# Kernel tuning notes

Hardware: AMD Instinct MI355X
Metric: run time of the kernel (lower is better)

Reference implementation:

```python
import jax, jax.numpy as jnp
import numpy as np

B, L = 64, 2048
V, E, G = 30, 128, 8          # n_tokens, embedding_size, n_globals
C, F, O = 64, 128, 30         # res_channels, f_channels, n_outputs
K, ND = 2, 9                  # kernel_size, n_dilations
GE = G * E                    # flattened global embedding dim


def causal_conv(x, w, b, dilation):
    # x: [B,Cin,L], w: [Cout,Cin,K] -> [B,Cout,L], causal via left padding
    pad = (w.shape[-1] - 1) * dilation
    out = jax.lax.conv_general_dilated(
        x, w, window_strides=(1,), padding=[(pad, 0)],
        rhs_dilation=(dilation,), dimension_numbers=("NCH", "OIH", "NCH"))
    return out + b[None, :, None]


def setup_inputs() -> dict:
    key = jax.random.key(0)
    ks = jax.random.split(key, 20)
    s = 0.05
    inp = {
        "input_tensor": jax.random.randint(ks[0], (B, L), 0, V),
        "global_input": jax.random.randint(ks[1], (B, G), 0, V),
        "emb_table": jax.random.normal(ks[2], (V, E), jnp.float32) * s,
        "w_causal": jax.random.normal(ks[3], (C, E, K), jnp.float32) * s,
        "b_causal": jnp.zeros((C,), jnp.float32),
        "w_f": jax.random.normal(ks[4], (ND, C, C, K), jnp.float32) * s,
        "b_f": jnp.zeros((ND, C), jnp.float32),
        "w_g": jax.random.normal(ks[5], (ND, C, C, K), jnp.float32) * s,
        "b_g": jnp.zeros((ND, C), jnp.float32),
        "wl_f": jax.random.normal(ks[6], (ND, C, GE), jnp.float32) * s,
        "bl_f": jnp.zeros((ND, C), jnp.float32),
        "wl_g": jax.random.normal(ks[7], (ND, C, GE), jnp.float32) * s,
        "bl_g": jnp.zeros((ND, C), jnp.float32),
        "w_res": jax.random.normal(ks[8], (ND, C, C), jnp.float32) * s,
        "b_res": jnp.zeros((ND, C), jnp.float32),
        "w_fin1": jax.random.normal(ks[9], (F, C), jnp.float32) * s,
        "b_fin1": jnp.zeros((F,), jnp.float32),
        "w_fin2": jax.random.normal(ks[10], (O, F), jnp.float32) * s,
        "b_fin2": jnp.zeros((O,), jnp.float32),
    }
    return inp


def reference(input_tensor, global_input, emb_table, w_causal, b_causal,
              w_f, b_f, w_g, b_g, wl_f, bl_f, wl_g, bl_g,
              w_res, b_res, w_fin1, b_fin1, w_fin2, b_fin2):
    # padding_idx=0: row 0 is zero and receives no gradient
    table = emb_table.at[0].set(0.0)
    emb = table[input_tensor]                     # [B,L,E]
    emb_g = table[global_input].reshape(B, GE)    # [B,G*E]
    x = jnp.transpose(emb, (0, 2, 1))             # [B,E,L]
    res = causal_conv(x, w_causal, b_causal, 1)   # [B,C,L]
    skips = jnp.zeros_like(res)
    for i in range(ND):
        d = 2 ** (i + 1)
        h_f = emb_g @ wl_f[i].T + bl_f[i]         # [B,C]
        h_g = emb_g @ wl_g[i].T + bl_g[i]
        x_f = causal_conv(res, w_f[i], b_f[i], d) + h_f[:, :, None]
        x_g = causal_conv(res, w_g[i], b_g[i], d) + h_g[:, :, None]
        z = jnp.tanh(x_f) * jax.nn.sigmoid(x_g)   # gated activation
        skip = jnp.einsum("oc,bcl->bol", w_res[i], z) + b_res[i][None, :, None]
        res = res + skip
        skips = skips + skip
    out = jax.nn.relu(skips)
    out = jnp.einsum("fc,bcl->bfl", w_fin1, out) + b_fin1[None, :, None]
    out = jax.nn.relu(out)
    out = jnp.einsum("of,bfl->bol", w_fin2, out) + b_fin2[None, :, None]
    return out
```

## Files before the change

### kernel.cpp

```cpp
#include <hip/hip_runtime.h>
#include <stdint.h>

#define Bz 64
#define Lz 2048
#define Vz 30
#define Ez 128
#define Gz 8
#define Cz 64
#define Fz 128
#define Oz 30
#define NDz 9

typedef __attribute__((ext_vector_type(8))) short short8;
typedef __attribute__((ext_vector_type(4))) float floatx4;

#define MFMA16 __builtin_amdgcn_mfma_f32_16x16x32_bf16

__device__ __forceinline__ uint16_t f2bf(float f) {
    uint32_t u = __float_as_uint(f);
    u += 0x7fffu + ((u >> 16) & 1u);
    return (uint16_t)(u >> 16);
}
__device__ __forceinline__ uint32_t bfround(float f) {
    uint32_t u = __float_as_uint(f);
    return u + 0x7fffu + ((u >> 16) & 1u);
}
__device__ __forceinline__ uint32_t pack2(float lo, float hi) {
    return __builtin_amdgcn_perm(bfround(hi), bfround(lo), 0x07060302u);
}
__device__ __forceinline__ float bf2f(uint32_t u) {
    return __uint_as_float(u << 16);
}
__device__ __forceinline__ float gatefn(float f, float g) {
    float a = __expf(2.f * f);
    float b = __expf(-g);
    float ap1 = a + 1.f;
    return (a - 1.f) * __builtin_amdgcn_rcpf(fmaf(ap1, b, ap1));
}

#define N_WB   (NDz * 128 * 128)
#define N_WR   (NDz * 64 * 64)
#define N_W1   (Fz * Cz)
#define N_W2   (32 * Fz)
#define N_PROJ (Vz * Cz)
#define N_WLB  (NDz * 128 * 1024)
#define N_EMB  (Bz * 1024)
#define N_BIAS (NDz * 128)

__global__ void pack_k(const float* __restrict__ w_f, const float* __restrict__ w_g,
                       const float* __restrict__ w_res, const float* __restrict__ w_fin1,
                       const float* __restrict__ w_fin2, const float* __restrict__ w_causal,
                       const float* __restrict__ table, const int* __restrict__ gin,
                       const float* __restrict__ wl_f, const float* __restrict__ wl_g,
                       const float* __restrict__ b_f, const float* __restrict__ b_g,
                       const float* __restrict__ bl_f, const float* __restrict__ bl_g,
                       uint16_t* __restrict__ WB, uint16_t* __restrict__ WrB,
                       uint16_t* __restrict__ W1B, uint16_t* __restrict__ W2B,
                       float* __restrict__ proj0, float* __restrict__ proj1,
                       uint16_t* __restrict__ WLB, uint16_t* __restrict__ embG,
                       float* __restrict__ biasrow) {
    int tid = blockIdx.x * 256 + threadIdx.x;
    if (tid < N_WB) {
        int i = tid >> 14, rem = tid & 16383, ch = rem >> 7, k = rem & 127;
        int kin = k & 63, tap = (k < 64) ? 1 : 0;
        float v = (ch < 64) ? w_f[((i * Cz + ch) * Cz + kin) * 2 + tap]
                            : w_g[((i * Cz + (ch - 64)) * Cz + kin) * 2 + tap];
        WB[tid] = f2bf(v);
        return;
    }
    tid -= N_WB;
    if (tid < N_WR) { WrB[tid] = f2bf(w_res[tid]); return; }
    tid -= N_WR;
    if (tid < N_W1) { W1B[tid] = f2bf(w_fin1[tid]); return; }
    tid -= N_W1;
    if (tid < N_W2) {
        int o = tid >> 7, f = tid & 127;
        W2B[tid] = f2bf(o < Oz ? w_fin2[o * Fz + f] : 0.f);
        return;
    }
    tid -= N_W2;
    if (tid < N_PROJ) {
        int v = tid >> 6, c = tid & 63;
        float s0 = 0.f, s1 = 0.f;
        if (v != 0) {
            for (int e = 0; e < Ez; e++) {
                float tv = table[v * Ez + e];
                s0 += w_causal[(c * Ez + e) * 2 + 0] * tv;
                s1 += w_causal[(c * Ez + e) * 2 + 1] * tv;
            }
        }
        proj0[tid] = s0; proj1[tid] = s1;
        return;
    }
    tid -= N_PROJ;
    if (tid < N_WLB) {
        int row = tid >> 10, j = tid & 1023;
        int i = row >> 7, rem = row & 127, fg = rem >> 6, c = rem & 63;
        const float* wl = fg ? wl_g : wl_f;
        WLB[tid] = f2bf(wl[((size_t)(i * Cz + c)) * 1024 + j]);
        return;
    }
    tid -= N_WLB;
    if (tid < N_EMB) {
        int b = tid >> 10, j = tid & 1023;
        int g = j >> 7, e = j & 127;
        int v = gin[b * Gz + g];
        embG[tid] = f2bf(v ? table[v * Ez + e] : 0.f);
        return;
    }
    tid -= N_EMB;
    if (tid < N_BIAS) {
        int i = tid >> 7, rem = tid & 127, fg = rem >> 6, c = rem & 63;
        biasrow[tid] = (fg ? b_g : b_f)[i * Cz + c] + (fg ? bl_g : bl_f)[i * Cz + c];
    }
}

__global__ __launch_bounds__(256) void hgemm_k(
    const uint16_t* __restrict__ WLB, const uint16_t* __restrict__ embG,
    const float* __restrict__ biasrow, float* __restrict__ hhT) {
    int tx = threadIdx.x, lane = tx & 63, wave = tx >> 6;
    int nl = lane & 15, quad = lane >> 4;
    int row0 = blockIdx.x * 64 + wave * 16;
    floatx4 acc[4];
    float bv[4];
#pragma unroll
    for (int r = 0; r < 4; r++) bv[r] = biasrow[row0 + quad * 4 + r];
#pragma unroll
    for (int nt = 0; nt < 4; nt++)
#pragma unroll
        for (int r = 0; r < 4; r++) acc[nt][r] = bv[r];
    const uint16_t* ap = WLB + (size_t)(row0 + nl) * 1024 + quad * 8;
#pragma unroll 4
    for (int ks = 0; ks < 32; ks++) {
        short8 a = *(const short8*)(ap + ks * 32);
#pragma unroll
        for (int nt = 0; nt < 4; nt++) {
            short8 bb = *(const short8*)(embG + (size_t)(nt * 16 + nl) * 1024 + ks * 32 + quad * 8);
            acc[nt] = MFMA16(a, bb, acc[nt], 0, 0, 0);
        }
    }
#pragma unroll
    for (int nt = 0; nt < 4; nt++)
#pragma unroll
        for (int r = 0; r < 4; r++)
            hhT[(size_t)(row0 + quad * 4 + r) * 64 + nt * 16 + nl] = acc[nt][r];
}

__global__ __launch_bounds__(256) void init_k(
    const int* __restrict__ tok, const float* __restrict__ b_causal,
    const float* __restrict__ proj0, const float* __restrict__ proj1,
    uint16_t* __restrict__ res) {
    int tx = threadIdx.x;
    int q = tx & 15, tl = tx >> 4;
    int b = blockIdx.y;
    int t = blockIdx.x * 16 + tl;
    int v1 = tok[b * Lz + t];
    int v0 = (t > 0) ? tok[b * Lz + t - 1] : 0;
    float4 p1 = ((const float4*)(proj1 + v1 * Cz))[q];
    float4 p0 = ((const float4*)(proj0 + v0 * Cz))[q];
    float4 bc = ((const float4*)b_causal)[q];
    float rx = p1.x + p0.x + bc.x, ry = p1.y + p0.y + bc.y;
    float rz = p1.z + p0.z + bc.z, rw = p1.w + p0.w + bc.w;
    *(uint2*)(res + ((size_t)(b * Lz + t)) * Cz + q * 4) =
        make_uint2(pack2(rx, ry), pack2(rz, rw));
}

__global__ __launch_bounds__(256, 2) void fused_k(
    const uint16_t* __restrict__ rin, uint16_t* __restrict__ rout,
    const uint16_t* __restrict__ WB, const uint16_t* __restrict__ WrB,
    const float* __restrict__ hhT, const float* __restrict__ b_res) {
    __shared__ __align__(16) uint16_t R[256 * 72];
    __shared__ __align__(16) uint16_t Zb[256 * 72];
    int tx = threadIdx.x;
    int lane = tx & 63, wave = tx >> 6;
    int nl = lane & 15, quad = lane >> 4;
    int b = blockIdx.y, t0 = blockIdx.x * 128;
    const uint16_t* rb16 = rin + ((size_t)b * Lz) * Cz;

    if (t0 != 0) {
        const uint16_t* src = rb16 + (size_t)(t0 - 128) * Cz;
#pragma unroll
        for (int it = 0; it < 8; it++) {
            int id = it * 256 + tx, row = id >> 3, c8 = id & 7;
            uint4 v = *(const uint4*)(src + (size_t)row * Cz + c8 * 8);
            *(uint4*)(R + row * 72 + c8 * 8) = v;
        }
    } else {
#pragma unroll
        for (int it = 0; it < 8; it++) {
            int id = it * 256 + tx, row = id >> 3, c8 = id & 7;
            int t = row - 128;
            uint4 v = make_uint4(0u, 0u, 0u, 0u);
            if (t >= 0) v = *(const uint4*)(rb16 + (size_t)t * Cz + c8 * 8);
            *(uint4*)(R + row * 72 + c8 * 8) = v;
        }
    }
    floatx4 ss[8];
#pragma unroll
    for (int j = 0; j < 8; j++)
#pragma unroll
        for (int r = 0; r < 4; r++) ss[j][r] = 0.f;
    __syncthreads();

    const int chq = wave * 16 + quad * 4;
    const int NT0[6] = {0, 0, 0, 1, 3, 7};

#pragma unroll
    for (int l = 0; l < 6; l++) {
        const int d = 2 << l;
        const int nt0 = NT0[l];
        const uint16_t* wf = WB + l * 16384 + (wave * 16 + nl) * 128 + quad * 8;
        short8 AF[4], AG[4];
#pragma unroll
        for (int ks = 0; ks < 4; ks++) {
            AF[ks] = *(const short8*)(wf + ks * 32);
            AG[ks] = *(const short8*)(wf + 64 * 128 + ks * 32);
        }
        const uint16_t* wr = WrB + l * 4096 + (wave * 16 + nl) * 64 + quad * 8;
        short8 AR0 = *(const short8*)(wr);
        short8 AR1 = *(const short8*)(wr + 32);
        float hfv[4], hgv[4], brv[4];
        const float* hp = hhT + ((size_t)(l * 128 + wave * 16 + quad * 4)) * 64 + b;
#pragma unroll
        for (int r = 0; r < 4; r++) { hfv[r] = hp[r * 64]; hgv[r] = hp[4096 + r * 64]; }
        const float* brp = b_res + l * Cz + wave * 16 + quad * 4;
#pragma unroll
        for (int r = 0; r < 4; r++) brv[r] = brp[r];

#pragma unroll
        for (int nt = 0; nt < 16; nt++) {
            if (nt < nt0) continue;
            int rowa = nt * 16 + nl;
            int rowb = rowa - d; rowb = rowb < 0 ? 0 : rowb;
            const uint16_t* ra = R + rowa * 72 + quad * 8;
            const uint16_t* rb = R + rowb * 72 + quad * 8;
            short8 b0 = *(const short8*)(ra);
            short8 b1 = *(const short8*)(ra + 32);
            short8 b2 = *(const short8*)(rb);
            short8 b3 = *(const short8*)(rb + 32);
            floatx4 aF, aG;
#pragma unroll
            for (int r = 0; r < 4; r++) { aF[r] = hfv[r]; aG[r] = hgv[r]; }
            aF = MFMA16(AF[0], b0, aF, 0, 0, 0); aG = MFMA16(AG[0], b0, aG, 0, 0, 0);
            aF = MFMA16(AF[1], b1, aF, 0, 0, 0); aG = MFMA16(AG[1], b1, aG, 0, 0, 0);
            aF = MFMA16(AF[2], b2, aF, 0, 0, 0); aG = MFMA16(AG[2], b2, aG, 0, 0, 0);
            aF = MFMA16(AF[3], b3, aF, 0, 0, 0); aG = MFMA16(AG[3], b3, aG, 0, 0, 0);
            float z0 = gatefn(aF[0], aG[0]);
            float z1 = gatefn(aF[1], aG[1]);
            float z2 = gatefn(aF[2], aG[2]);
            float z3 = gatefn(aF[3], aG[3]);
            *(uint2*)(Zb + rowa * 72 + chq) = make_uint2(pack2(z0, z1), pack2(z2, z3));
        }
        __syncthreads();

        if (t0 != 0) {
#pragma unroll
            for (int nt = 0; nt < 16; nt++) {
                if (nt < nt0) continue;
                int pos = nt * 16 + nl;
                const uint16_t* zp = Zb + pos * 72 + quad * 8;
                floatx4 a2;
#pragma unroll
                for (int r = 0; r < 4; r++) a2[r] = brv[r];
                a2 = MFMA16(AR0, *(const short8*)zp, a2, 0, 0, 0);
                a2 = MFMA16(AR1, *(const short8*)(zp + 32), a2, 0, 0, 0);
                uint16_t* rp = R + pos * 72 + chq;
                uint2 oldp = *(uint2*)rp;
                float n0 = bf2f(oldp.x & 0xffffu) + a2[0];
                float n1 = bf2f(oldp.x >> 16) + a2[1];
                float n2 = bf2f(oldp.y & 0xffffu) + a2[2];
                float n3 = bf2f(oldp.y >> 16) + a2[3];
                *(uint2*)rp = make_uint2(pack2(n0, n1), pack2(n2, n3));
                if (nt >= 8) {
#pragma unroll
                    for (int r = 0; r < 4; r++) ss[nt - 8][r] += a2[r];
                }
            }
        } else {
#pragma unroll
            for (int nt = 0; nt < 16; nt++) {
                if (nt < nt0) continue;
                int pos = nt * 16 + nl;
                const uint16_t* zp = Zb + pos * 72 + quad * 8;
                floatx4 a2;
#pragma unroll
                for (int r = 0; r < 4; r++) a2[r] = brv[r];
                a2 = MFMA16(AR0, *(const short8*)zp, a2, 0, 0, 0);
                a2 = MFMA16(AR1, *(const short8*)(zp + 32), a2, 0, 0, 0);
                int t = pos - 128;
                uint16_t* rp = R + pos * 72 + chq;
                uint2 oldp = *(uint2*)rp;
                bool ok = (t >= 0);
                float n0 = ok ? bf2f(oldp.x & 0xffffu) + a2[0] : 0.f;
                float n1 = ok ? bf2f(oldp.x >> 16) + a2[1] : 0.f;
                float n2 = ok ? bf2f(oldp.y & 0xffffu) + a2[2] : 0.f;
                float n3 = ok ? bf2f(oldp.y >> 16) + a2[3] : 0.f;
                *(uint2*)rp = make_uint2(pack2(n0, n1), pack2(n2, n3));
                if (nt >= 8) {
#pragma unroll
                    for (int r = 0; r < 4; r++) ss[nt - 8][r] += a2[r];
                }
            }
        }
        __syncthreads();
    }

    uint16_t* ro = rout + ((size_t)b * Lz) * Cz;
#pragma unroll
    for (int j = 0; j < 8; j++) {
        size_t off = (size_t)(t0 + j * 16 + nl) * Cz + chq;
        uint2 rv = *(const uint2*)(rb16 + off);
        float n0 = bf2f(rv.x & 0xffffu) + ss[j][0];
        float n1 = bf2f(rv.x >> 16) + ss[j][1];
        float n2 = bf2f(rv.y & 0xffffu) + ss[j][2];
        float n3 = bf2f(rv.y >> 16) + ss[j][3];
        *(uint2*)(ro + off) = make_uint2(pack2(n0, n1), pack2(n2, n3));
    }
}

__global__ __launch_bounds__(256, 4) void layer_k(
    const uint16_t* __restrict__ rin, uint16_t* __restrict__ rout,
    const uint16_t* __restrict__ WBl, const uint16_t* __restrict__ WrBl,
    const float* __restrict__ hhT, const float* __restrict__ b_res,
    int i, int d) {
    __shared__ __align__(16) uint16_t X[64 * 136];
    __shared__ __align__(16) uint16_t Z[64 * 72];
    int tx = threadIdx.x;
    int lane = tx & 63, wave = tx >> 6;
    int nl = lane & 15, quad = lane >> 4;
    int b = blockIdx.y, t0 = blockIdx.x * 64;
    const uint16_t* rb16 = rin + ((size_t)b * Lz) * Cz;

#pragma unroll
    for (int it = 0; it < 2; it++) {
        int id = it * 256 + tx, row = id >> 3, c8 = id & 7;
        uint4 v = *(const uint4*)(rb16 + (size_t)(t0 + row) * Cz + c8 * 8);
        *(uint4*)(X + row * 136 + c8 * 8) = v;
    }
#pragma unroll
    for (int it = 0; it < 2; it++) {
        int id = it * 256 + tx, row = id >> 3, c8 = id & 7;
        int tb = t0 + row - d;
        uint4 v = make_uint4(0u, 0u, 0u, 0u);
        if (tb >= 0) v = *(const uint4*)(rb16 + (size_t)tb * Cz + c8 * 8);
        *(uint4*)(X + row * 136 + 64 + c8 * 8) = v;
    }

    short8 AF[4], AG[4], AR[2];
    {
        const uint16_t* wf = WBl + (wave * 16 + nl) * 128 + quad * 8;
#pragma unroll
        for (int ks = 0; ks < 4; ks++) {
            AF[ks] = *(const short8*)(wf + ks * 32);
            AG[ks] = *(const short8*)(wf + 64 * 128 + ks * 32);
        }
        const uint16_t* wr = WrBl + (wave * 16 + nl) * 64 + quad * 8;
#pragma unroll
        for (int ks = 0; ks < 2; ks++) AR[ks] = *(const short8*)(wr + ks * 32);
    }
    float hfv[4], hgv[4], brv[4];
    {
        const float* hp = hhT + ((size_t)(i * 128 + wave * 16 + quad * 4)) * 64 + b;
#pragma unroll
        for (int r = 0; r < 4; r++) {
            hfv[r] = hp[r * 64];
            hgv[r] = hp[4096 + r * 64];
        }
        const float* brp = b_res + i * Cz + wave * 16 + quad * 4;
#pragma unroll
        for (int r = 0; r < 4; r++) brv[r] = brp[r];
    }
    __syncthreads();

    floatx4 accF[4], accG[4];
#pragma unroll
    for (int nt = 0; nt < 4; nt++)
#pragma unroll
        for (int r = 0; r < 4; r++) { accF[nt][r] = hfv[r]; accG[nt][r] = hgv[r]; }
#pragma unroll
    for (int nt = 0; nt < 4; nt++) {
        const uint16_t* xp = X + (nt * 16 + nl) * 136 + quad * 8;
#pragma unroll
        for (int ks = 0; ks < 4; ks++) {
            short8 bf = *(const short8*)(xp + ks * 32);
            accF[nt] = MFMA16(AF[ks], bf, accF[nt], 0, 0, 0);
            accG[nt] = MFMA16(AG[ks], bf, accG[nt], 0, 0, 0);
        }
    }

    int chq = wave * 16 + quad * 4;
#pragma unroll
    for (int nt = 0; nt < 4; nt++) {
        int pos = nt * 16 + nl;
        float z0 = gatefn(accF[nt][0], accG[nt][0]);
        float z1 = gatefn(accF[nt][1], accG[nt][1]);
        float z2 = gatefn(accF[nt][2], accG[nt][2]);
        float z3 = gatefn(accF[nt][3], accG[nt][3]);
        *(uint2*)(Z + pos * 72 + chq) = make_uint2(pack2(z0, z1), pack2(z2, z3));
    }
    __syncthreads();

    floatx4 acc2[4];
#pragma unroll
    for (int nt = 0; nt < 4; nt++)
#pragma unroll
        for (int r = 0; r < 4; r++) acc2[nt][r] = brv[r];
#pragma unroll
    for (int nt = 0; nt < 4; nt++) {
        const uint16_t* zp = Z + (nt * 16 + nl) * 72 + quad * 8;
        acc2[nt] = MFMA16(AR[0], *(const short8*)zp, acc2[nt], 0, 0, 0);
        acc2[nt] = MFMA16(AR[1], *(const short8*)(zp + 32), acc2[nt], 0, 0, 0);
    }

    uint16_t* ro = rout + ((size_t)b * Lz) * Cz;
#pragma unroll
    for (int nt = 0; nt < 4; nt++) {
        size_t off = (size_t)(t0 + nt * 16 + nl) * Cz + chq;
        uint2 rv = *(const uint2*)(rb16 + off);
        float n0 = bf2f(rv.x & 0xffffu) + acc2[nt][0];
        float n1 = bf2f(rv.x >> 16) + acc2[nt][1];
        float n2 = bf2f(rv.y & 0xffffu) + acc2[nt][2];
        float n3 = bf2f(rv.y >> 16) + acc2[nt][3];
        *(uint2*)(ro + off) = make_uint2(pack2(n0, n1), pack2(n2, n3));
    }
}

__global__ __launch_bounds__(256, 3) void final_k(
    const uint16_t* __restrict__ res0, const uint16_t* __restrict__ resF,
    const uint16_t* __restrict__ W1B, const uint16_t* __restrict__ W2B,
    const float* __restrict__ b_fin1, const float* __restrict__ b_fin2,
    float* __restrict__ out) {
    __shared__ __align__(16) uint16_t S[128 * 72];
    __shared__ __align__(16) uint16_t Mi[128 * 136];
    int tx = threadIdx.x;
    int lane = tx & 63, wave = tx >> 6;
    int nl = lane & 15, quad = lane >> 4;
    int b = blockIdx.y, t0 = blockIdx.x * 128;
    const uint16_t* r0 = res0 + ((size_t)b * Lz) * Cz;
    const uint16_t* rF = resF + ((size_t)b * Lz) * Cz;

    short8 A1[2][2], A2[2][4];
#pragma unroll
    for (int mt = 0; mt < 2; mt++) {
        const uint16_t* w1 = W1B + (wave * 32 + mt * 16 + nl) * 64 + quad * 8;
#pragma unroll
        for (int ks = 0; ks < 2; ks++) A1[mt][ks] = *(const short8*)(w1 + ks * 32);
        const uint16_t* w2 = W2B + (mt * 16 + nl) * 128 + quad * 8;
#pragma unroll
        for (int ks = 0; ks < 4; ks++) A2[mt][ks] = *(const short8*)(w2 + ks * 32);
    }
#pragma unroll
    for (int it = 0; it < 4; it++) {
        int id = it * 256 + tx, row = id >> 3, c8 = id & 7;
        uint4 fv = *(const uint4*)(rF + (size_t)(t0 + row) * Cz + c8 * 8);
        uint4 ov = *(const uint4*)(r0 + (size_t)(t0 + row) * Cz + c8 * 8);
        float s0 = fmaxf(bf2f(fv.x & 0xffffu) - bf2f(ov.x & 0xffffu), 0.f);
        float s1 = fmaxf(bf2f(fv.x >> 16) - bf2f(ov.x >> 16), 0.f);
        float s2 = fmaxf(bf2f(fv.y & 0xffffu) - bf2f(ov.y & 0xffffu), 0.f);
        float s3 = fmaxf(bf2f(fv.y >> 16) - bf2f(ov.y >> 16), 0.f);
        float s4 = fmaxf(bf2f(fv.z & 0xffffu) - bf2f(ov.z & 0xffffu), 0.f);
        float s5 = fmaxf(bf2f(fv.z >> 16) - bf2f(ov.z >> 16), 0.f);
        float s6 = fmaxf(bf2f(fv.w & 0xffffu) - bf2f(ov.w & 0xffffu), 0.f);
        float s7 = fmaxf(bf2f(fv.w >> 16) - bf2f(ov.w >> 16), 0.f);
        *(uint4*)(S + row * 72 + c8 * 8) =
            make_uint4(pack2(s0, s1), pack2(s2, s3), pack2(s4, s5), pack2(s6, s7));
    }
    __syncthreads();

    floatx4 accM[2][8];
    float b1v[2][4];
#pragma unroll
    for (int mt = 0; mt < 2; mt++)
#pragma unroll
        for (int r = 0; r < 4; r++) b1v[mt][r] = b_fin1[wave * 32 + mt * 16 + quad * 4 + r];
#pragma unroll
    for (int mt = 0; mt < 2; mt++)
#pragma unroll
        for (int nt = 0; nt < 8; nt++)
#pragma unroll
            for (int r = 0; r < 4; r++) accM[mt][nt][r] = b1v[mt][r];
#pragma unroll
    for (int nt = 0; nt < 8; nt++) {
        const uint16_t* sp = S + (nt * 16 + nl) * 72 + quad * 8;
#pragma unroll
        for (int ks = 0; ks < 2; ks++) {
            short8 s = *(const short8*)(sp + ks * 32);
            accM[0][nt] = MFMA16(A1[0][ks], s, accM[0][nt], 0, 0, 0);
            accM[1][nt] = MFMA16(A1[1][ks], s, accM[1][nt], 0, 0, 0);
        }
    }
#pragma unroll
    for (int mt = 0; mt < 2; mt++)
#pragma unroll
        for (int nt = 0; nt < 8; nt++) {
            int pos = nt * 16 + nl;
            int fq = wave * 32 + mt * 16 + quad * 4;
            float m0 = fmaxf(accM[mt][nt][0], 0.f), m1 = fmaxf(accM[mt][nt][1], 0.f);
            float m2 = fmaxf(accM[mt][nt][2], 0.f), m3 = fmaxf(accM[mt][nt][3], 0.f);
            *(uint2*)(Mi + pos * 136 + fq) = make_uint2(pack2(m0, m1), pack2(m2, m3));
        }
    __syncthreads();

    floatx4 accO[2][2];
#pragma unroll
    for (int mt = 0; mt < 2; mt++)
#pragma unroll
        for (int r = 0; r < 4; r++) {
            int o = mt * 16 + quad * 4 + r;
            float bo = (o < Oz) ? b_fin2[o] : 0.f;
            accO[mt][0][r] = bo; accO[mt][1][r] = bo;
        }
#pragma unroll
    for (int ntl = 0; ntl < 2; ntl++) {
        int nt = wave * 2 + ntl;
        const uint16_t* mp = Mi + (nt * 16 + nl) * 136 + quad * 8;
#pragma unroll
        for (int ks = 0; ks < 4; ks++) {
            short8 m = *(const short8*)(mp + ks * 32);
            accO[0][ntl] = MFMA16(A2[0][ks], m, accO[0][ntl], 0, 0, 0);
            accO[1][ntl] = MFMA16(A2[1][ks], m, accO[1][ntl], 0, 0, 0);
        }
    }
#pragma unroll
    for (int mt = 0; mt < 2; mt++)
#pragma unroll
        for (int ntl = 0; ntl < 2; ntl++)
#pragma unroll
            for (int r = 0; r < 4; r++) {
                int o = mt * 16 + quad * 4 + r;
                if (o < Oz)
                    out[((size_t)b * Oz + o) * Lz + t0 + (wave * 2 + ntl) * 16 + nl] =
                        accO[mt][ntl][r];
            }
}

extern "C" void kernel_launch(void* const* d_in, const int* in_sizes, int n_in,
                              void* d_out, int out_size, void* d_ws, size_t ws_size,
                              hipStream_t stream) {
    const int*   tok      = (const int*)d_in[0];
    const int*   gin      = (const int*)d_in[1];
    const float* table    = (const float*)d_in[2];
    const float* w_causal = (const float*)d_in[3];
    const float* b_causal = (const float*)d_in[4];
    const float* w_f      = (const float*)d_in[5];
    const float* b_f      = (const float*)d_in[6];
    const float* w_g      = (const float*)d_in[7];
    const float* b_g      = (const float*)d_in[8];
    const float* wl_f     = (const float*)d_in[9];
    const float* bl_f     = (const float*)d_in[10];
    const float* wl_g     = (const float*)d_in[11];
    const float* bl_g     = (const float*)d_in[12];
    const float* w_res    = (const float*)d_in[13];
    const float* b_res    = (const float*)d_in[14];
    const float* w_fin1   = (const float*)d_in[15];
    const float* b_fin1   = (const float*)d_in[16];
    const float* w_fin2   = (const float*)d_in[17];
    const float* b_fin2   = (const float*)d_in[18];
    float* out = (float*)d_out;

    const size_t NRES = (size_t)Bz * Lz * Cz;
    uint16_t* u16 = (uint16_t*)d_ws;
    uint16_t* resA = u16;
    uint16_t* resB = resA + NRES;
    uint16_t* resC = resB + NRES;
    uint16_t* WB   = resC + NRES;
    uint16_t* WrB  = WB + N_WB;
    uint16_t* W1B  = WrB + N_WR;
    uint16_t* W2B  = W1B + N_W1;
    uint16_t* WLB  = W2B + N_W2;
    uint16_t* embG = WLB + N_WLB;
    float* hhT     = (float*)(embG + N_EMB);
    float* proj0   = hhT + 73728;
    float* proj1   = proj0 + N_PROJ;
    float* biasrow = proj1 + N_PROJ;

    int npack = N_WB + N_WR + N_W1 + N_W2 + N_PROJ + N_WLB + N_EMB + N_BIAS;
    pack_k<<<(npack + 255) / 256, 256, 0, stream>>>(
        w_f, w_g, w_res, w_fin1, w_fin2, w_causal, table, gin,
        wl_f, wl_g, b_f, b_g, bl_f, bl_g,
        WB, WrB, W1B, W2B, proj0, proj1, WLB, embG, biasrow);
    hgemm_k<<<18, 256, 0, stream>>>(WLB, embG, biasrow, hhT);
    init_k<<<dim3(Lz / 16, Bz), 256, 0, stream>>>(tok, b_causal, proj0, proj1, resA);

    fused_k<<<dim3(Lz / 128, Bz), 256, 0, stream>>>(resA, resB, WB, WrB, hhT, b_res);
    layer_k<<<dim3(Lz / 64, Bz), 256, 0, stream>>>(
        resB, resC, WB + (size_t)6 * 16384, WrB + (size_t)6 * 4096, hhT, b_res, 6, 128);
    layer_k<<<dim3(Lz / 64, Bz), 256, 0, stream>>>(
        resC, resB, WB + (size_t)7 * 16384, WrB + (size_t)7 * 4096, hhT, b_res, 7, 256);
    layer_k<<<dim3(Lz / 64, Bz), 256, 0, stream>>>(
        resB, resC, WB + (size_t)8 * 16384, WrB + (size_t)8 * 4096, hhT, b_res, 8, 512);
    final_k<<<dim3(Lz / 128, Bz), 256, 0, stream>>>(resA, resC, W1B, W2B,
                                                    b_fin1, b_fin2, out);
}
```

Measured before the change: 300.6 us.

## Switch residual stream and MFMA operands from bf16 to fp16 with packed conversions

Stores weights and the residual and activation buffers as fp16 instead of bf16 and uses the fp16 MFMA variant. Manual bf16 rounding and unpacking are replaced by hardware packed convert (cvt_pkrtz) and packed fp16 adds, which cuts ALU work in the epilogues. The skipped-tile table NT0 and the row clamping are also adjusted so fewer tiles are computed in early layers. The trade-off is fp16's narrower range and round-toward-zero conversion, plus a changed boundary computation that must still be correct.

```diff
diff --git a/kernel.cpp b/kernel.cpp
--- a/kernel.cpp
+++ b/kernel.cpp
@@ -12,24 +12,31 @@
 #define NDz 9
 
 typedef __attribute__((ext_vector_type(8))) short short8;
+typedef _Float16 half8 __attribute__((ext_vector_type(8)));
+typedef __fp16 fp16x2 __attribute__((ext_vector_type(2)));
 typedef __attribute__((ext_vector_type(4))) float floatx4;
 
-#define MFMA16 __builtin_amdgcn_mfma_f32_16x16x32_bf16
+#define MFMA16B __builtin_amdgcn_mfma_f32_16x16x32_bf16
+#define MFMA16H __builtin_amdgcn_mfma_f32_16x16x32_f16
 
 __device__ __forceinline__ uint16_t f2bf(float f) {
     uint32_t u = __float_as_uint(f);
     u += 0x7fffu + ((u >> 16) & 1u);
     return (uint16_t)(u >> 16);
 }
-__device__ __forceinline__ uint32_t bfround(float f) {
-    uint32_t u = __float_as_uint(f);
-    return u + 0x7fffu + ((u >> 16) & 1u);
-}
-__device__ __forceinline__ uint32_t pack2(float lo, float hi) {
-    return __builtin_amdgcn_perm(bfround(hi), bfround(lo), 0x07060302u);
-}
-__device__ __forceinline__ float bf2f(uint32_t u) {
-    return __uint_as_float(u << 16);
+__device__ __forceinline__ uint16_t f2h(float f) {
+    return __builtin_bit_cast(uint16_t, (_Float16)f);
+}
+__device__ __forceinline__ uint32_t pk2h(float lo, float hi) {
+    fp16x2 h = __builtin_amdgcn_cvt_pkrtz(lo, hi);
+    return __builtin_bit_cast(uint32_t, h);
+}
+__device__ __forceinline__ uint32_t pkadd(uint32_t oldbits, float a, float b) {
+    fp16x2 h = __builtin_bit_cast(fp16x2, oldbits) + __builtin_amdgcn_cvt_pkrtz(a, b);
+    return __builtin_bit_cast(uint32_t, h);
+}
+__device__ __forceinline__ float h2f(uint32_t u16bits) {
+    return (float)__builtin_bit_cast(_Float16, (uint16_t)u16bits);
 }
 __device__ __forceinline__ float gatefn(float f, float g) {
     float a = __expf(2.f * f);
@@ -65,17 +72,17 @@
         int kin = k & 63, tap = (k < 64) ? 1 : 0;
         float v = (ch < 64) ? w_f[((i * Cz + ch) * Cz + kin) * 2 + tap]
                             : w_g[((i * Cz + (ch - 64)) * Cz + kin) * 2 + tap];
-        WB[tid] = f2bf(v);
+        WB[tid] = f2h(v);
         return;
     }
     tid -= N_WB;
-    if (tid < N_WR) { WrB[tid] = f2bf(w_res[tid]); return; }
+    if (tid < N_WR) { WrB[tid] = f2h(w_res[tid]); return; }
     tid -= N_WR;
-    if (tid < N_W1) { W1B[tid] = f2bf(w_fin1[tid]); return; }
+    if (tid < N_W1) { W1B[tid] = f2h(w_fin1[tid]); return; }
     tid -= N_W1;
     if (tid < N_W2) {
         int o = tid >> 7, f = tid & 127;
-        W2B[tid] = f2bf(o < Oz ? w_fin2[o * Fz + f] : 0.f);
+        W2B[tid] = f2h(o < Oz ? w_fin2[o * Fz + f] : 0.f);
         return;
     }
     tid -= N_W2;
@@ -136,7 +143,7 @@
 #pragma unroll
         for (int nt = 0; nt < 4; nt++) {
             short8 bb = *(const short8*)(embG + (size_t)(nt * 16 + nl) * 1024 + ks * 32 + quad * 8);
-            acc[nt] = MFMA16(a, bb, acc[nt], 0, 0, 0);
+            acc[nt] = MFMA16B(a, bb, acc[nt], 0, 0, 0);
         }
     }
 #pragma unroll
@@ -162,7 +169,7 @@
     float rx = p1.x + p0.x + bc.x, ry = p1.y + p0.y + bc.y;
     float rz = p1.z + p0.z + bc.z, rw = p1.w + p0.w + bc.w;
     *(uint2*)(res + ((size_t)(b * Lz + t)) * Cz + q * 4) =
-        make_uint2(pack2(rx, ry), pack2(rz, rw));
+        make_uint2(pk2h(rx, ry), pk2h(rz, rw));
 }
 
 __global__ __launch_bounds__(256, 2) void fused_k(
@@ -203,22 +210,22 @@
     __syncthreads();
 
     const int chq = wave * 16 + quad * 4;
-    const int NT0[6] = {0, 0, 0, 1, 3, 7};
+    const int NT0[6] = {0, 0, 1, 2, 4, 8};
 
 #pragma unroll
     for (int l = 0; l < 6; l++) {
         const int d = 2 << l;
         const int nt0 = NT0[l];
         const uint16_t* wf = WB + l * 16384 + (wave * 16 + nl) * 128 + quad * 8;
-        short8 AF[4], AG[4];
+        half8 AF[4], AG[4];
 #pragma unroll
         for (int ks = 0; ks < 4; ks++) {
-            AF[ks] = *(const short8*)(wf + ks * 32);
-            AG[ks] = *(const short8*)(wf + 64 * 128 + ks * 32);
+            AF[ks] = *(const half8*)(wf + ks * 32);
+            AG[ks] = *(const half8*)(wf + 64 * 128 + ks * 32);
         }
         const uint16_t* wr = WrB + l * 4096 + (wave * 16 + nl) * 64 + quad * 8;
-        short8 AR0 = *(const short8*)(wr);
-        short8 AR1 = *(const short8*)(wr + 32);
+        half8 AR0 = *(const half8*)(wr);
+        half8 AR1 = *(const half8*)(wr + 32);
         float hfv[4], hgv[4], brv[4];
         const float* hp = hhT + ((size_t)(l * 128 + wave * 16 + quad * 4)) * 64 + b;
 #pragma unroll
@@ -231,25 +238,26 @@
         for (int nt = 0; nt < 16; nt++) {
             if (nt < nt0) continue;
             int rowa = nt * 16 + nl;
-            int rowb = rowa - d; rowb = rowb < 0 ? 0 : rowb;
+            int rowb = rowa - d;
+            if (nt * 16 < d) rowb = rowb < 0 ? 0 : rowb;
             const uint16_t* ra = R + rowa * 72 + quad * 8;
             const uint16_t* rb = R + rowb * 72 + quad * 8;
-            short8 b0 = *(const short8*)(ra);
-            short8 b1 = *(const short8*)(ra + 32);
-            short8 b2 = *(const short8*)(rb);
-            short8 b3 = *(const short8*)(rb + 32);
+            half8 b0 = *(const half8*)(ra);
+            half8 b1 = *(const half8*)(ra + 32);
+            half8 b2 = *(const half8*)(rb);
+            half8 b3 = *(const half8*)(rb + 32);
             floatx4 aF, aG;
 #pragma unroll
             for (int r = 0; r < 4; r++) { aF[r] = hfv[r]; aG[r] = hgv[r]; }
-            aF = MFMA16(AF[0], b0, aF, 0, 0, 0); aG = MFMA16(AG[0], b0, aG, 0, 0, 0);
-            aF = MFMA16(AF[1], b1, aF, 0, 0, 0); aG = MFMA16(AG[1], b1, aG, 0, 0, 0);
-            aF = MFMA16(AF[2], b2, aF, 0, 0, 0); aG = MFMA16(AG[2], b2, aG, 0, 0, 0);
-            aF = MFMA16(AF[3], b3, aF, 0, 0, 0); aG = MFMA16(AG[3], b3, aG, 0, 0, 0);
+            aF = MFMA16H(AF[0], b0, aF, 0, 0, 0); aG = MFMA16H(AG[0], b0, aG, 0, 0, 0);
+            aF = MFMA16H(AF[1], b1, aF, 0, 0, 0); aG = MFMA16H(AG[1], b1, aG, 0, 0, 0);
+            aF = MFMA16H(AF[2], b2, aF, 0, 0, 0); aG = MFMA16H(AG[2], b2, aG, 0, 0, 0);
+            aF = MFMA16H(AF[3], b3, aF, 0, 0, 0); aG = MFMA16H(AG[3], b3, aG, 0, 0, 0);
             float z0 = gatefn(aF[0], aG[0]);
             float z1 = gatefn(aF[1], aG[1]);
             float z2 = gatefn(aF[2], aG[2]);
             float z3 = gatefn(aF[3], aG[3]);
-            *(uint2*)(Zb + rowa * 72 + chq) = make_uint2(pack2(z0, z1), pack2(z2, z3));
+            *(uint2*)(Zb + rowa * 72 + chq) = make_uint2(pk2h(z0, z1), pk2h(z2, z3));
         }
         __syncthreads();
 
@@ -262,15 +270,12 @@
                 floatx4 a2;
 #pragma unroll
                 for (int r = 0; r < 4; r++) a2[r] = brv[r];
-                a2 = MFMA16(AR0, *(const short8*)zp, a2, 0, 0, 0);
-                a2 = MFMA16(AR1, *(const short8*)(zp + 32), a2, 0, 0, 0);
+                a2 = MFMA16H(AR0, *(const half8*)zp, a2, 0, 0, 0);
+                a2 = MFMA16H(AR1, *(const half8*)(zp + 32), a2, 0, 0, 0);
                 uint16_t* rp = R + pos * 72 + chq;
                 uint2 oldp = *(uint2*)rp;
-                float n0 = bf2f(oldp.x & 0xffffu) + a2[0];
-                float n1 = bf2f(oldp.x >> 16) + a2[1];
-                float n2 = bf2f(oldp.y & 0xffffu) + a2[2];
-                float n3 = bf2f(oldp.y >> 16) + a2[3];
-                *(uint2*)rp = make_uint2(pack2(n0, n1), pack2(n2, n3));
+                *(uint2*)rp = make_uint2(pkadd(oldp.x, a2[0], a2[1]),
+                                         pkadd(oldp.y, a2[2], a2[3]));
                 if (nt >= 8) {
 #pragma unroll
                     for (int r = 0; r < 4; r++) ss[nt - 8][r] += a2[r];
@@ -285,17 +290,14 @@
                 floatx4 a2;
 #pragma unroll
                 for (int r = 0; r < 4; r++) a2[r] = brv[r];
-                a2 = MFMA16(AR0, *(const short8*)zp, a2, 0, 0, 0);
-                a2 = MFMA16(AR1, *(const short8*)(zp + 32), a2, 0, 0, 0);
-                int t = pos - 128;
+                a2 = MFMA16H(AR0, *(const half8*)zp, a2, 0, 0, 0);
+                a2 = MFMA16H(AR1, *(const half8*)(zp + 32), a2, 0, 0, 0);
+                bool ok = (pos >= 128);
                 uint16_t* rp = R + pos * 72 + chq;
                 uint2 oldp = *(uint2*)rp;
-                bool ok = (t >= 0);
-                float n0 = ok ? bf2f(oldp.x & 0xffffu) + a2[0] : 0.f;
-                float n1 = ok ? bf2f(oldp.x >> 16) + a2[1] : 0.f;
-                float n2 = ok ? bf2f(oldp.y & 0xffffu) + a2[2] : 0.f;
-                float n3 = ok ? bf2f(oldp.y >> 16) + a2[3] : 0.f;
-                *(uint2*)rp = make_uint2(pack2(n0, n1), pack2(n2, n3));
+                uint32_t ux = ok ? pkadd(oldp.x, a2[0], a2[1]) : 0u;
+                uint32_t uy = ok ? pkadd(oldp.y, a2[2], a2[3]) : 0u;
+                *(uint2*)rp = make_uint2(ux, uy);
                 if (nt >= 8) {
 #pragma unroll
                     for (int r = 0; r < 4; r++) ss[nt - 8][r] += a2[r];
@@ -310,11 +312,8 @@
     for (int j = 0; j < 8; j++) {
         size_t off = (size_t)(t0 + j * 16 + nl) * Cz + chq;
         uint2 rv = *(const uint2*)(rb16 + off);
-        float n0 = bf2f(rv.x & 0xffffu) + ss[j][0];
-        float n1 = bf2f(rv.x >> 16) + ss[j][1];
-        float n2 = bf2f(rv.y & 0xffffu) + ss[j][2];
-        float n3 = bf2f(rv.y >> 16) + ss[j][3];
-        *(uint2*)(ro + off) = make_uint2(pack2(n0, n1), pack2(n2, n3));
+        *(uint2*)(ro + off) = make_uint2(pkadd(rv.x, ss[j][0], ss[j][1]),
+                                         pkadd(rv.y, ss[j][2], ss[j][3]));
     }
 }
 
@@ -346,17 +345,17 @@
         *(uint4*)(X + row * 136 + 64 + c8 * 8) = v;
     }
 
-    short8 AF[4], AG[4], AR[2];
+    half8 AF[4], AG[4], AR[2];
     {
         const uint16_t* wf = WBl + (wave * 16 + nl) * 128 + quad * 8;
 #pragma unroll
         for (int ks = 0; ks < 4; ks++) {
-            AF[ks] = *(const short8*)(wf + ks * 32);
-            AG[ks] = *(const short8*)(wf + 64 * 128 + ks * 32);
+            AF[ks] = *(const half8*)(wf + ks * 32);
+            AG[ks] = *(const half8*)(wf + 64 * 128 + ks * 32);
         }
         const uint16_t* wr = WrBl + (wave * 16 + nl) * 64 + quad * 8;
 #pragma unroll
-        for (int ks = 0; ks < 2; ks++) AR[ks] = *(const short8*)(wr + ks * 32);
+        for (int ks = 0; ks < 2; ks++) AR[ks] = *(const half8*)(wr + ks * 32);
     }
     float hfv[4], hgv[4], brv[4];
     {
@@ -382,9 +381,9 @@
         const uint16_t* xp = X + (nt * 16 + nl) * 136 + quad * 8;
 #pragma unroll
         for (int ks = 0; ks < 4; ks++) {
-            short8 bf = *(const short8*)(xp + ks * 32);
-            accF[nt] = MFMA16(AF[ks], bf, accF[nt], 0, 0, 0);
-            accG[nt] = MFMA16(AG[ks], bf, accG[nt], 0, 0, 0);
+            half8 bf = *(const half8*)(xp + ks * 32);
+            accF[nt] = MFMA16H(AF[ks], bf, accF[nt], 0, 0, 0);
+            accG[nt] = MFMA16H(AG[ks], bf, accG[nt], 0, 0, 0);
         }
     }
 
@@ -396,7 +395,7 @@
         float z1 = gatefn(accF[nt][1], accG[nt][1]);
         float z2 = gatefn(accF[nt][2], accG[nt][2]);
         float z3 = gatefn(accF[nt][3], accG[nt][3]);
-        *(uint2*)(Z + pos * 72 + chq) = make_uint2(pack2(z0, z1), pack2(z2, z3));
+        *(uint2*)(Z + pos * 72 + chq) = make_uint2(pk2h(z0, z1), pk2h(z2, z3));
     }
     __syncthreads();
 
@@ -408,8 +407,8 @@
 #pragma unroll
     for (int nt = 0; nt < 4; nt++) {
         const uint16_t* zp = Z + (nt * 16 + nl) * 72 + quad * 8;
-        acc2[nt] = MFMA16(AR[0], *(const short8*)zp, acc2[nt], 0, 0, 0);
-        acc2[nt] = MFMA16(AR[1], *(const short8*)(zp + 32), acc2[nt], 0, 0, 0);
+        acc2[nt] = MFMA16H(AR[0], *(const half8*)zp, acc2[nt], 0, 0, 0);
+        acc2[nt] = MFMA16H(AR[1], *(const half8*)(zp + 32), acc2[nt], 0, 0, 0);
     }
 
     uint16_t* ro = rout + ((size_t)b * Lz) * Cz;
@@ -417,11 +416,8 @@
     for (int nt = 0; nt < 4; nt++) {
         size_t off = (size_t)(t0 + nt * 16 + nl) * Cz + chq;
         uint2 rv = *(const uint2*)(rb16 + off);
-        float n0 = bf2f(rv.x & 0xffffu) + acc2[nt][0];
-        float n1 = bf2f(rv.x >> 16) + acc2[nt][1];
-        float n2 = bf2f(rv.y & 0xffffu) + acc2[nt][2];
-        float n3 = bf2f(rv.y >> 16) + acc2[nt][3];
-        *(uint2*)(ro + off) = make_uint2(pack2(n0, n1), pack2(n2, n3));
+        *(uint2*)(ro + off) = make_uint2(pkadd(rv.x, acc2[nt][0], acc2[nt][1]),
+                                         pkadd(rv.y, acc2[nt][2], acc2[nt][3]));
     }
 }
 
@@ -439,31 +435,31 @@
     const uint16_t* r0 = res0 + ((size_t)b * Lz) * Cz;
     const uint16_t* rF = resF + ((size_t)b * Lz) * Cz;
 
-    short8 A1[2][2], A2[2][4];
+    half8 A1[2][2], A2[2][4];
 #pragma unroll
     for (int mt = 0; mt < 2; mt++) {
         const uint16_t* w1 = W1B + (wave * 32 + mt * 16 + nl) * 64 + quad * 8;
 #pragma unroll
-        for (int ks = 0; ks < 2; ks++) A1[mt][ks] = *(const short8*)(w1 + ks * 32);
+        for (int ks = 0; ks < 2; ks++) A1[mt][ks] = *(const half8*)(w1 + ks * 32);
         const uint16_t* w2 = W2B + (mt * 16 + nl) * 128 + quad * 8;
 #pragma unroll
-        for (int ks = 0; ks < 4; ks++) A2[mt][ks] = *(const short8*)(w2 + ks * 32);
+        for (int ks = 0; ks < 4; ks++) A2[mt][ks] = *(const half8*)(w2 + ks * 32);
     }
 #pragma unroll
     for (int it = 0; it < 4; it++) {
         int id = it * 256 + tx, row = id >> 3, c8 = id & 7;
         uint4 fv = *(const uint4*)(rF + (size_t)(t0 + row) * Cz + c8 * 8);
         uint4 ov = *(const uint4*)(r0 + (size_t)(t0 + row) * Cz + c8 * 8);
-        float s0 = fmaxf(bf2f(fv.x & 0xffffu) - bf2f(ov.x & 0xffffu), 0.f);
-        float s1 = fmaxf(bf2f(fv.x >> 16) - bf2f(ov.x >> 16), 0.f);
-        float s2 = fmaxf(bf2f(fv.y & 0xffffu) - bf2f(ov.y & 0xffffu), 0.f);
-        float s3 = fmaxf(bf2f(fv.y >> 16) - bf2f(ov.y >> 16), 0.f);
-        float s4 = fmaxf(bf2f(fv.z & 0xffffu) - bf2f(ov.z & 0xffffu), 0.f);
-        float s5 = fmaxf(bf2f(fv.z >> 16) - bf2f(ov.z >> 16), 0.f);
-        float s6 = fmaxf(bf2f(fv.w & 0xffffu) - bf2f(ov.w & 0xffffu), 0.f);
-        float s7 = fmaxf(bf2f(fv.w >> 16) - bf2f(ov.w >> 16), 0.f);
+        float s0 = fmaxf(h2f(fv.x) - h2f(ov.x), 0.f);
+        float s1 = fmaxf(h2f(fv.x >> 16) - h2f(ov.x >> 16), 0.f);
+        float s2 = fmaxf(h2f(fv.y) - h2f(ov.y), 0.f);
+        float s3 = fmaxf(h2f(fv.y >> 16) - h2f(ov.y >> 16), 0.f);
+        float s4 = fmaxf(h2f(fv.z) - h2f(ov.z), 0.f);
+        float s5 = fmaxf(h2f(fv.z >> 16) - h2f(ov.z >> 16), 0.f);
+        float s6 = fmaxf(h2f(fv.w) - h2f(ov.w), 0.f);
+        float s7 = fmaxf(h2f(fv.w >> 16) - h2f(ov.w >> 16), 0.f);
         *(uint4*)(S + row * 72 + c8 * 8) =
-            make_uint4(pack2(s0, s1), pack2(s2, s3), pack2(s4, s5), pack2(s6, s7));
+            make_uint4(pk2h(s0, s1), pk2h(s2, s3), pk2h(s4, s5), pk2h(s6, s7));
     }
     __syncthreads();
 
@@ -484,9 +480,9 @@
         const uint16_t* sp = S + (nt * 16 + nl) * 72 + quad * 8;
 #pragma unroll
         for (int ks = 0; ks < 2; ks++) {
-            short8 s = *(const short8*)(sp + ks * 32);
-            accM[0][nt] = MFMA16(A1[0][ks], s, accM[0][nt], 0, 0, 0);
-            accM[1][nt] = MFMA16(A1[1][ks], s, accM[1][nt], 0, 0, 0);
+            half8 s = *(const half8*)(sp + ks * 32);
+            accM[0][nt] = MFMA16H(A1[0][ks], s, accM[0][nt], 0, 0, 0);
+            accM[1][nt] = MFMA16H(A1[1][ks], s, accM[1][nt], 0, 0, 0);
         }
     }
 #pragma unroll
@@ -497,7 +493,7 @@
             int fq = wave * 32 + mt * 16 + quad * 4;
             float m0 = fmaxf(accM[mt][nt][0], 0.f), m1 = fmaxf(accM[mt][nt][1], 0.f);
             float m2 = fmaxf(accM[mt][nt][2], 0.f), m3 = fmaxf(accM[mt][nt][3], 0.f);
-            *(uint2*)(Mi + pos * 136 + fq) = make_uint2(pack2(m0, m1), pack2(m2, m3));
+            *(uint2*)(Mi + pos * 136 + fq) = make_uint2(pk2h(m0, m1), pk2h(m2, m3));
         }
     __syncthreads();
 
@@ -516,9 +512,9 @@
         const uint16_t* mp = Mi + (nt * 16 + nl) * 136 + quad * 8;
 #pragma unroll
         for (int ks = 0; ks < 4; ks++) {
-            short8 m = *(const short8*)(mp + ks * 32);
-            accO[0][ntl] = MFMA16(A2[0][ks], m, accO[0][ntl], 0, 0, 0);
-            accO[1][ntl] = MFMA16(A2[1][ks], m, accO[1][ntl], 0, 0, 0);
+            half8 m = *(const half8*)(mp + ks * 32);
+            accO[0][ntl] = MFMA16H(A2[0][ks], m, accO[0][ntl], 0, 0, 0);
+            accO[1][ntl] = MFMA16H(A2[1][ks], m, accO[1][ntl], 0, 0, 0);
         }
     }
 #pragma unroll
```

After: 289.9 us. 3.6% less time.
